# Performance work log

Measured on AMD Instinct MI355X. Metric: run time of the kernel, lower is better.

The kernel has to match this reference:

```python
import jax, jax.numpy as jnp
import numpy as np

N, D = 8192, 1024
MAX_REP = 8

def setup_inputs() -> dict:
    key = jax.random.key(0)
    k1, k2 = jax.random.split(key)
    encoder_h = jax.random.normal(k1, (N, D), dtype=jnp.float32)
    repeats = jax.random.randint(k2, (N,), 0, MAX_REP, dtype=jnp.int32)
    return {"encoder_h": encoder_h, "repeats": repeats}

def reference(encoder_h, repeats):
    # Variable-length repeat_interleave along axis 0.
    # Equivalent to tf tile+sequence_mask+boolean_mask+reshape in the original,
    # but expressed as a single cumsum-index gather (no max_repeat-sized blowup).
    repeats = repeats.astype(jnp.int32)
    total = int(jnp.sum(repeats))  # dynamic output length (data-dependent)
    csum = jnp.cumsum(repeats)                     # [N]
    # row index for each output slot: searchsorted maps output position -> source row
    idx = jnp.searchsorted(csum, jnp.arange(total, dtype=jnp.int32), side='right')  # [total]
    return encoder_h[idx]                          # [total, D]
```

## Files before the change

### kernel.cpp

```cpp
#include <hip/hip_runtime.h>


typedef float nfloat4 __attribute__((ext_vector_type(4)));

#define CHUNK 4
#define BLOCK 256

__global__ __launch_bounds__(BLOCK)
void spread_fused_kernel(const nfloat4* __restrict__ h,
                         const int* __restrict__ repeats,
                         nfloat4* __restrict__ out,
                         int n, int d4 ) {
    const int rbase = blockIdx.x * CHUNK;
    const int t = threadIdx.x;
    const int lane = t & 63;
    const int wave = t >> 6;

    __shared__ int wpart[BLOCK / 64];
    int local = 0;
    {
        const int nq = rbase >> 2;
        const int4* rp4 = (const int4*)repeats;
        for (int q = t; q < nq; q += BLOCK) {
            const int4 v = rp4[q];
            local += v.x + v.y + v.z + v.w;
        }
    }
#pragma unroll
    for (int off = 32; off > 0; off >>= 1)
        local += __shfl_down(local, off, 64);
    if (lane == 0) wpart[wave] = local;
    __syncthreads();
    const int obase = wpart[0] + wpart[1] + wpart[2] + wpart[3];

    int reps[CHUNK];
    if (rbase + CHUNK <= n) {
        const int4 r4 = *(const int4*)(repeats + rbase);
        reps[0] = r4.x; reps[1] = r4.y; reps[2] = r4.z; reps[3] = r4.w;
    } else {
#pragma unroll
        for (int j = 0; j < CHUNK; ++j)
            reps[j] = (rbase + j < n) ? repeats[rbase + j] : 0;
    }
    int offs[CHUNK];
    offs[0] = obase;
#pragma unroll
    for (int j = 1; j < CHUNK; ++j) offs[j] = offs[j - 1] + reps[j - 1];

    for (int i = t; i < d4; i += BLOCK) {
        nfloat4 v[CHUNK];
#pragma unroll
        for (int j = 0; j < CHUNK; ++j) {
            const int row = rbase + j;
            v[j] = (row < n) ? h[(size_t)row * d4 + i] : nfloat4{0, 0, 0, 0};
        }
#pragma unroll
        for (int j = 0; j < CHUNK; ++j) {
            const int r = reps[j];
            nfloat4* __restrict__ dst = out + (size_t)offs[j] * d4 + i;
            for (int k = 0; k < r; ++k) {
                dst[(size_t)k * d4] = v[j];
            }
        }
    }
}

extern "C" void kernel_launch(void* const* d_in, const int* in_sizes, int n_in,
                              void* d_out, int out_size, void* d_ws, size_t ws_size,
                              hipStream_t stream) {
    const float* encoder_h = (const float*)d_in[0];
    const int*   repeats   = (const int*)d_in[1];
    float*       out       = (float*)d_out;

    const int n = in_sizes[1];
    const int d = in_sizes[0] / n;

    const int nblocks = (n + CHUNK - 1) / CHUNK;
    spread_fused_kernel<<<nblocks, BLOCK, 0, stream>>>(
        (const nfloat4*)encoder_h, repeats, (nfloat4*)out, n, d / 4);
}
```

Baseline: 144.1 us.

## Switch to persistent blocks pulling row chunks from an atomic ticket counter

Replaces the one-block-per-4-row-chunk launch with a capped grid of persistent blocks. Each block repeatedly grabs the next chunk through an atomicAdd on a workspace counter, which is reset by a memset before the launch. The goal is to balance the uneven per-chunk write volume that the variable repeat counts create and to cut block launch overhead. It also skips loading source rows whose repeat count is zero. In exchange it adds an extra memset operation, an atomic and two block barriers per chunk, and it still recomputes the prefix sum from scratch for every chunk.

```diff
diff --git a/kernel.cpp b/kernel.cpp
--- a/kernel.cpp
+++ b/kernel.cpp
@@ -3,63 +3,70 @@
 
 typedef float nfloat4 __attribute__((ext_vector_type(4)));
 
+#define BLOCK 256
 #define CHUNK 4
-#define BLOCK 256
+#define NBLOCKS 1024
 
 __global__ __launch_bounds__(BLOCK)
-void spread_fused_kernel(const nfloat4* __restrict__ h,
-                         const int* __restrict__ repeats,
-                         nfloat4* __restrict__ out,
-                         int n, int d4 ) {
-    const int rbase = blockIdx.x * CHUNK;
+void spread_dynamic_kernel(const nfloat4* __restrict__ h,
+                           const int* __restrict__ repeats,
+                           nfloat4* __restrict__ out,
+                           int* __restrict__ ticket,
+                           int n, int d4 ) {
+    __shared__ int s_chunk;
+    __shared__ int wpart[BLOCK / 64];
     const int t = threadIdx.x;
     const int lane = t & 63;
     const int wave = t >> 6;
+    const int nchunks = (n + CHUNK - 1) / CHUNK;
+    const int4* rp4 = (const int4*)repeats;
 
-    __shared__ int wpart[BLOCK / 64];
-    int local = 0;
-    {
-        const int nq = rbase >> 2;
-        const int4* rp4 = (const int4*)repeats;
-        for (int q = t; q < nq; q += BLOCK) {
+    for (;;) {
+        if (t == 0) s_chunk = atomicAdd(ticket, 1);
+        __syncthreads();
+        const int c = s_chunk;
+        if (c >= nchunks) return;
+        const int rbase = c * CHUNK;
+
+        int local = 0;
+        for (int q = t; q < c; q += BLOCK) {
             const int4 v = rp4[q];
             local += v.x + v.y + v.z + v.w;
         }
-    }
 #pragma unroll
-    for (int off = 32; off > 0; off >>= 1)
-        local += __shfl_down(local, off, 64);
-    if (lane == 0) wpart[wave] = local;
-    __syncthreads();
-    const int obase = wpart[0] + wpart[1] + wpart[2] + wpart[3];
+        for (int off = 32; off > 0; off >>= 1)
+            local += __shfl_down(local, off, 64);
+        if (lane == 0) wpart[wave] = local;
+        __syncthreads();
+        const int obase = wpart[0] + wpart[1] + wpart[2] + wpart[3];
 
-    int reps[CHUNK];
-    if (rbase + CHUNK <= n) {
-        const int4 r4 = *(const int4*)(repeats + rbase);
-        reps[0] = r4.x; reps[1] = r4.y; reps[2] = r4.z; reps[3] = r4.w;
-    } else {
+        int reps[CHUNK];
+        if (rbase + CHUNK <= n) {
+            const int4 r4 = *(const int4*)(repeats + rbase);
+            reps[0] = r4.x; reps[1] = r4.y; reps[2] = r4.z; reps[3] = r4.w;
+        } else {
 #pragma unroll
-        for (int j = 0; j < CHUNK; ++j)
-            reps[j] = (rbase + j < n) ? repeats[rbase + j] : 0;
-    }
-    int offs[CHUNK];
-    offs[0] = obase;
+            for (int j = 0; j < CHUNK; ++j)
+                reps[j] = (rbase + j < n) ? repeats[rbase + j] : 0;
+        }
+        int offs[CHUNK];
+        offs[0] = obase;
 #pragma unroll
-    for (int j = 1; j < CHUNK; ++j) offs[j] = offs[j - 1] + reps[j - 1];
+        for (int j = 1; j < CHUNK; ++j) offs[j] = offs[j - 1] + reps[j - 1];
 
-    for (int i = t; i < d4; i += BLOCK) {
-        nfloat4 v[CHUNK];
+        for (int i = t; i < d4; i += BLOCK) {
+            nfloat4 v[CHUNK];
 #pragma unroll
-        for (int j = 0; j < CHUNK; ++j) {
-            const int row = rbase + j;
-            v[j] = (row < n) ? h[(size_t)row * d4 + i] : nfloat4{0, 0, 0, 0};
-        }
+            for (int j = 0; j < CHUNK; ++j) {
+                if (reps[j] > 0)
+                    v[j] = h[(size_t)(rbase + j) * d4 + i];
+            }
 #pragma unroll
-        for (int j = 0; j < CHUNK; ++j) {
-            const int r = reps[j];
-            nfloat4* __restrict__ dst = out + (size_t)offs[j] * d4 + i;
-            for (int k = 0; k < r; ++k) {
-                dst[(size_t)k * d4] = v[j];
+            for (int j = 0; j < CHUNK; ++j) {
+                const int r = reps[j];
+                nfloat4* __restrict__ dst = out + (size_t)offs[j] * d4 + i;
+                for (int k = 0; k < r; ++k)
+                    dst[(size_t)k * d4] = v[j];
             }
         }
     }
@@ -75,7 +82,11 @@
     const int n = in_sizes[1];
     const int d = in_sizes[0] / n;
 
-    const int nblocks = (n + CHUNK - 1) / CHUNK;
-    spread_fused_kernel<<<nblocks, BLOCK, 0, stream>>>(
-        (const nfloat4*)encoder_h, repeats, (nfloat4*)out, n, d / 4);
+    int* ticket = (int*)d_ws;
+    hipMemsetAsync(ticket, 0, sizeof(int), stream);
+
+    const int nchunks = (n + CHUNK - 1) / CHUNK;
+    const int grid = nchunks < NBLOCKS ? nchunks : NBLOCKS;
+    spread_dynamic_kernel<<<grid, BLOCK, 0, stream>>>(
+        (const nfloat4*)encoder_h, repeats, (nfloat4*)out, ticket, n, d / 4);
 }
```

Result: slower. 155.7 us (+8.1%).

## Assign one block per source row and skip rows with zero repeats

Applied to the files above, without the earlier changes.

Each block now handles a single source row instead of four. Blocks whose row has zero repeats exit early, skipping both the prefix-sum and the row read. A specialized kernel for D/4 == 256 has each thread load one float4 before the prefix reduction so the load overlaps with it. The cost is four times as many blocks, each repeating the prefix scan over the preceding repeats, which adds redundant reads of the repeats array.

```diff
diff --git a/kernel.cpp b/kernel.cpp
--- a/kernel.cpp
+++ b/kernel.cpp
@@ -3,29 +3,33 @@
 
 typedef float nfloat4 __attribute__((ext_vector_type(4)));
 
-#define CHUNK 4
 #define BLOCK 256
 
 __global__ __launch_bounds__(BLOCK)
-void spread_fused_kernel(const nfloat4* __restrict__ h,
-                         const int* __restrict__ repeats,
-                         nfloat4* __restrict__ out,
-                         int n, int d4 ) {
-    const int rbase = blockIdx.x * CHUNK;
+void spread_row_kernel(const nfloat4* __restrict__ h,
+                       const int* __restrict__ repeats,
+                       nfloat4* __restrict__ out,
+                       int d4 ) {
+    const int row = blockIdx.x;
     const int t = threadIdx.x;
+
+    const int r = repeats[row];
+    if (r == 0) return;
+
+    const nfloat4 v = h[(size_t)row * d4 + t];
+
+    const int nq = row >> 2;
+    const int4* rp4 = (const int4*)repeats;
+    int local = 0;
+    for (int q = t; q < nq; q += BLOCK) {
+        const int4 w = rp4[q];
+        local += w.x + w.y + w.z + w.w;
+    }
+    if (t < (row & 3)) local += repeats[(nq << 2) + t];
+
     const int lane = t & 63;
     const int wave = t >> 6;
-
     __shared__ int wpart[BLOCK / 64];
-    int local = 0;
-    {
-        const int nq = rbase >> 2;
-        const int4* rp4 = (const int4*)repeats;
-        for (int q = t; q < nq; q += BLOCK) {
-            const int4 v = rp4[q];
-            local += v.x + v.y + v.z + v.w;
-        }
-    }
 #pragma unroll
     for (int off = 32; off > 0; off >>= 1)
         local += __shfl_down(local, off, 64);
@@ -33,35 +37,45 @@
     __syncthreads();
     const int obase = wpart[0] + wpart[1] + wpart[2] + wpart[3];
 
-    int reps[CHUNK];
-    if (rbase + CHUNK <= n) {
-        const int4 r4 = *(const int4*)(repeats + rbase);
-        reps[0] = r4.x; reps[1] = r4.y; reps[2] = r4.z; reps[3] = r4.w;
-    } else {
+    nfloat4* __restrict__ dst = out + (size_t)obase * d4 + t;
+    for (int k = 0; k < r; ++k)
+        dst[(size_t)k * d4] = v;
+}
+
+__global__ __launch_bounds__(BLOCK)
+void spread_row_generic_kernel(const nfloat4* __restrict__ h,
+                               const int* __restrict__ repeats,
+                               nfloat4* __restrict__ out,
+                               int d4) {
+    const int row = blockIdx.x;
+    const int t = threadIdx.x;
+    const int r = repeats[row];
+    if (r == 0) return;
+
+    const int nq = row >> 2;
+    const int4* rp4 = (const int4*)repeats;
+    int local = 0;
+    for (int q = t; q < nq; q += BLOCK) {
+        const int4 w = rp4[q];
+        local += w.x + w.y + w.z + w.w;
+    }
+    if (t < (row & 3)) local += repeats[(nq << 2) + t];
+
+    const int lane = t & 63;
+    const int wave = t >> 6;
+    __shared__ int wpart[BLOCK / 64];
 #pragma unroll
-        for (int j = 0; j < CHUNK; ++j)
-            reps[j] = (rbase + j < n) ? repeats[rbase + j] : 0;
-    }
-    int offs[CHUNK];
-    offs[0] = obase;
-#pragma unroll
-    for (int j = 1; j < CHUNK; ++j) offs[j] = offs[j - 1] + reps[j - 1];
+    for (int off = 32; off > 0; off >>= 1)
+        local += __shfl_down(local, off, 64);
+    if (lane == 0) wpart[wave] = local;
+    __syncthreads();
+    const int obase = wpart[0] + wpart[1] + wpart[2] + wpart[3];
 
     for (int i = t; i < d4; i += BLOCK) {
-        nfloat4 v[CHUNK];
-#pragma unroll
-        for (int j = 0; j < CHUNK; ++j) {
-            const int row = rbase + j;
-            v[j] = (row < n) ? h[(size_t)row * d4 + i] : nfloat4{0, 0, 0, 0};
-        }
-#pragma unroll
-        for (int j = 0; j < CHUNK; ++j) {
-            const int r = reps[j];
-            nfloat4* __restrict__ dst = out + (size_t)offs[j] * d4 + i;
-            for (int k = 0; k < r; ++k) {
-                dst[(size_t)k * d4] = v[j];
-            }
-        }
+        const nfloat4 v = h[(size_t)row * d4 + i];
+        nfloat4* __restrict__ dst = out + (size_t)obase * d4 + i;
+        for (int k = 0; k < r; ++k)
+            dst[(size_t)k * d4] = v;
     }
 }
 
@@ -74,8 +88,13 @@
 
     const int n = in_sizes[1];
     const int d = in_sizes[0] / n;
+    const int d4 = d / 4;
 
-    const int nblocks = (n + CHUNK - 1) / CHUNK;
-    spread_fused_kernel<<<nblocks, BLOCK, 0, stream>>>(
-        (const nfloat4*)encoder_h, repeats, (nfloat4*)out, n, d / 4);
+    if (d4 == BLOCK) {
+        spread_row_kernel<<<n, BLOCK, 0, stream>>>(
+            (const nfloat4*)encoder_h, repeats, (nfloat4*)out, d4);
+    } else {
+        spread_row_generic_kernel<<<n, BLOCK, 0, stream>>>(
+            (const nfloat4*)encoder_h, repeats, (nfloat4*)out, d4);
+    }
 }
```

New measurement: 144.1 us. Within noise of the previous version (+0.0%).
